# Kernel tuning notes

Hardware: AMD Instinct MI355X
Metric: run time of the kernel (lower is better)

Reference implementation:

```python
import jax, jax.numpy as jnp
import numpy as np

S, B, D, H = 512, 16, 512, 8  # seq_len, batch, d_model, n_heads
DH = D // H


def setup_inputs() -> dict:
    key = jax.random.key(0)
    k1, k2, k3, k4, k5 = jax.random.split(key, 5)
    x = jax.random.normal(k1, (S, B, D), dtype=jnp.float32)
    # nn.MultiheadAttention params: packed in_proj [3D, D], out_proj [D, D]
    W_in = jax.random.normal(k2, (3 * D, D), dtype=jnp.float32) * (D ** -0.5)
    b_in = jax.random.normal(k3, (3 * D,), dtype=jnp.float32) * 0.02
    W_out = jax.random.normal(k4, (D, D), dtype=jnp.float32) * (D ** -0.5)
    b_out = jax.random.normal(k5, (D,), dtype=jnp.float32) * 0.02
    return {"x": x, "W_in": W_in, "b_in": b_in, "W_out": W_out, "b_out": b_out}


def _mha(q_in, k_in, v_in, W_in, b_in, W_out, b_out):
    """torch.nn.MultiheadAttention (batch_first=False, eval mode). Inputs: (S, B, D)."""
    Wq, Wk, Wv = jnp.split(W_in, 3, axis=0)
    bq, bk, bv = jnp.split(b_in, 3)

    def heads(t):  # (S, B, D) -> (B, H, S, DH)
        s, b, _ = t.shape
        return t.reshape(s, b, H, DH).transpose(1, 2, 0, 3)

    q = heads(q_in @ Wq.T + bq) * (DH ** -0.5)
    k = heads(k_in @ Wk.T + bk)
    v = heads(v_in @ Wv.T + bv)
    attn = jax.nn.softmax(jnp.einsum('bhsd,bhtd->bhst', q, k), axis=-1)
    o = jnp.einsum('bhst,bhtd->bhsd', attn, v)          # (B, H, S, DH)
    o = o.transpose(2, 0, 1, 3).reshape(q_in.shape)      # (S, B, D)
    return o @ W_out.T + b_out


def reference(x, W_in, b_in, W_out, b_out):
    ch = jnp.arange(x.shape[-1])  # channel indices of last dim

    def step(acc, i):
        # x_i: only channel i kept (mirrors x_i[..., i] = x[..., i])
        x_i = jnp.where(ch == i, x, 0.0)
        # x_i_prime = where(x_i == 0, x, 0): x with channel i zeroed (where nonzero)
        x_ip = jnp.where(x_i == 0.0, x, 0.0)
        out = _mha(x_i, x_ip, x_ip, W_in, b_in, W_out, b_out)
        return acc + out, None

    # loop runs x.size(1) times, exactly as the torch code
    acc, _ = jax.lax.scan(step, jnp.zeros_like(x), jnp.arange(x.shape[1]))
    return acc
```

## Files before the change

kernel.cpp:

```cpp
#include <hip/hip_runtime.h>

#define S_LEN 512
#define BATCH 16
#define DMODEL 512
#define NHEAD 8
#define DH 64
#define NI 16

typedef float f32x4 __attribute__((ext_vector_type(4)));
typedef float f32x2 __attribute__((ext_vector_type(2)));
typedef short s16x8 __attribute__((ext_vector_type(8)));

__device__ __forceinline__ unsigned short f2bf(float f){
  unsigned int u = __float_as_uint(f);
  u += 0x7FFFu + ((u >> 16) & 1u);
  return (unsigned short)(u >> 16);
}

__device__ __forceinline__ void async16(const unsigned short* g, unsigned short* l){
  __builtin_amdgcn_global_load_lds(
      (const __attribute__((address_space(1))) unsigned int*)g,
      (__attribute__((address_space(3))) unsigned int*)l, 16, 0, 0);
}

template<int CTRL>
__device__ __forceinline__ float dppAdd(float x){
  int v = __builtin_amdgcn_update_dpp(0, __float_as_int(x), CTRL, 0xF, 0xF, true);
  return x + __int_as_float(v);
}

__device__ __forceinline__ void plswap32(float &a, float &b){
  asm("v_permlane32_swap_b32 %0, %1" : "+v"(a), "+v"(b));
}
__device__ __forceinline__ void plswap16(float &a, float &b){
  asm("v_permlane16_swap_b32 %0, %1" : "+v"(a), "+v"(b));
}
__device__ __forceinline__ unsigned int cvtpk_bf16(float lo, float hi){
  unsigned int r;
  asm("v_cvt_pk_bf16_f32 %0, %1, %2" : "=v"(r) : "v"(lo), "v"(hi));
  return r;
}

__global__ void k_prep(const float* __restrict__ x, unsigned short* __restrict__ xb,
                       float* __restrict__ zcol){
  int tid = blockIdx.x * 256 + threadIdx.x;
  float4 v = reinterpret_cast<const float4*>(x)[tid];
  ushort4 o;
  o.x = f2bf(v.x); o.y = f2bf(v.y); o.z = f2bf(v.z); o.w = f2bf(v.w);
  reinterpret_cast<ushort4*>(xb)[tid] = o;
  int d0 = (tid & 127) * 4;
  if (d0 < 16){
    int row = tid >> 7;
    int t = row >> 4, b = row & 15;
    zcol[(size_t)(b * 16 + d0 + 0) * 512 + t] = v.x;
    zcol[(size_t)(b * 16 + d0 + 1) * 512 + t] = v.y;
    zcol[(size_t)(b * 16 + d0 + 2) * 512 + t] = v.z;
    zcol[(size_t)(b * 16 + d0 + 3) * 512 + t] = v.w;
  }
}

__global__ void k_wcvt(const float* __restrict__ Win, const float* __restrict__ Wout,
                       unsigned short* __restrict__ Winb, unsigned short* __restrict__ Wob){
  int bidx = blockIdx.x;
  if (bidx < 768){
    int t = bidx * 256 + threadIdx.x;
    float4 v = reinterpret_cast<const float4*>(Win)[t];
    ushort4 o;
    o.x = f2bf(v.x); o.y = f2bf(v.y); o.z = f2bf(v.z); o.w = f2bf(v.w);
    reinterpret_cast<ushort4*>(Winb)[t] = o;
  } else {
    int t = (bidx - 768) * 256 + threadIdx.x;
    float4 v = reinterpret_cast<const float4*>(Wout)[t];
    ushort4 o;
    o.x = f2bf(v.x); o.y = f2bf(v.y); o.z = f2bf(v.z); o.w = f2bf(v.w);
    reinterpret_cast<ushort4*>(Wob)[t] = o;
  }
}

__global__ __launch_bounds__(256) void k_kv2(const unsigned short* __restrict__ xb,
    const unsigned short* __restrict__ Winb, const float* __restrict__ b_in,
    float* __restrict__ Kf, unsigned short* __restrict__ Vfb){
  __shared__ unsigned short As[2][128 * 32];
  __shared__ unsigned short Bs[2][128 * 32];
  int tid = threadIdx.x;
  int w = tid >> 6, l = tid & 63;
  int ln = l & 15, kb = l >> 4;
  int wr = w >> 1, wc = w & 1;
  int m0 = blockIdx.x * 128;
  int n0 = blockIdx.y * 128;
  const unsigned short* Brow = Winb + (size_t)512 * DMODEL;

  f32x4 acc[4][4];
  #pragma unroll
  for (int mi = 0; mi < 4; ++mi)
    #pragma unroll
    for (int nj = 0; nj < 4; ++nj) acc[mi][nj] = (f32x4){0.f,0.f,0.f,0.f};

  int c0 = tid, c1 = 256 + tid;
  int r0 = c0 >> 2, q0 = c0 & 3, r1 = c1 >> 2, q1 = c1 & 3;
  int lb0 = (w * 64) * 8, lb1 = (256 + w * 64) * 8;

  #define STAGE_KV(kt, buf) do { int k0 = (kt) * 32;                                   \
    async16(xb   + (size_t)(m0 + r0) * DMODEL + k0 + q0 * 8, &As[buf][lb0]);           \
    async16(xb   + (size_t)(m0 + r1) * DMODEL + k0 + q1 * 8, &As[buf][lb1]);           \
    async16(Brow + (size_t)(n0 + r0) * DMODEL + k0 + q0 * 8, &Bs[buf][lb0]);           \
    async16(Brow + (size_t)(n0 + r1) * DMODEL + k0 + q1 * 8, &Bs[buf][lb1]);           \
  } while(0)

  STAGE_KV(0, 0);
  __syncthreads();
  int cur = 0;
  for (int kt = 0; kt < 16; ++kt){
    if (kt < 15) STAGE_KV(kt + 1, cur ^ 1);
    const unsigned short* Ab = &As[cur][(wr * 64 + ln) * 32 + kb * 8];
    const unsigned short* Bb = &Bs[cur][(wc * 64 + ln) * 32 + kb * 8];
    s16x8 af[4], bf[4];
    #pragma unroll
    for (int mi = 0; mi < 4; ++mi) af[mi] = *reinterpret_cast<const s16x8*>(Ab + mi * 16 * 32);
    #pragma unroll
    for (int nj = 0; nj < 4; ++nj) bf[nj] = *reinterpret_cast<const s16x8*>(Bb + nj * 16 * 32);
    #pragma unroll
    for (int mi = 0; mi < 4; ++mi)
      #pragma unroll
      for (int nj = 0; nj < 4; ++nj)
        acc[mi][nj] = __builtin_amdgcn_mfma_f32_16x16x32_bf16(af[mi], bf[nj], acc[mi][nj], 0, 0, 0);
    __syncthreads();
    cur ^= 1;
  }
  #undef STAGE_KV

  #pragma unroll
  for (int nj = 0; nj < 4; ++nj){
    int n = n0 + wc * 64 + nj * 16 + ln;
    float bias = b_in[512 + n];
    #pragma unroll
    for (int mi = 0; mi < 4; ++mi){
      #pragma unroll
      for (int r = 0; r < 4; ++r){
        int m = m0 + wr * 64 + mi * 16 + kb * 4 + r;
        float v = acc[mi][nj][r] + bias;
        if (n < DMODEL) Kf[(size_t)m * DMODEL + n] = v;
        else            Vfb[(size_t)m * DMODEL + (n - DMODEL)] = f2bf(v);
      }
    }
  }
}

__global__ void k_tr(const unsigned short* __restrict__ Vfb, unsigned short* __restrict__ VfT){
  __shared__ unsigned short tile[32][34];
  int b = blockIdx.z; int t0 = blockIdx.x * 32; int d0 = blockIdx.y * 32;
  int tx = threadIdx.x & 31, ty = threadIdx.x >> 5;
  #pragma unroll
  for (int k = 0; k < 4; ++k){
    int row = ty + 8 * k;
    tile[row][tx] = Vfb[(size_t)((t0 + row) * BATCH + b) * DMODEL + d0 + tx];
  }
  __syncthreads();
  #pragma unroll
  for (int k = 0; k < 4; ++k){
    int row = ty + 8 * k;
    VfT[(size_t)b * (DMODEL * S_LEN) + (size_t)(d0 + row) * S_LEN + t0 + tx] = tile[tx][row];
  }
}

__global__ __launch_bounds__(256) void k_gh(const float* __restrict__ W_in,
    const float* __restrict__ b_in, const float* __restrict__ Kf,
    const float* __restrict__ zcol, float* __restrict__ G, float* __restrict__ H){
  const float SCALE = 0.18033688011112042f;
  int bh = blockIdx.x >> 1, th = blockIdx.x & 1;
  int b = bh >> 3, h = bh & 7;
  __shared__ float u[64][17];
  __shared__ float cvec[64];
  __shared__ float alpha[16], beta[16];
  int tid = threadIdx.x;
  for (int idx = tid; idx < 1024; idx += 256){
    int d = idx >> 4, i = idx & 15;
    u[d][i] = W_in[(size_t)(h * 64 + d) * DMODEL + i];
  }
  if (tid < 64) cvec[tid] = b_in[h * 64 + tid];
  __syncthreads();
  if (tid < 16){
    float a = 0.f, be = 0.f;
    for (int d = 0; d < 64; ++d){
      float wk = W_in[(size_t)(512 + h * 64 + d) * DMODEL + tid];
      a  += u[d][tid] * wk;
      be += cvec[d] * wk;
    }
    alpha[tid] = a; beta[tid] = be;
  }
  __syncthreads();
  int t = th * 256 + tid;
  float K[64];
  const float* kp = Kf + (size_t)(t * BATCH + b) * DMODEL + h * 64;
  #pragma unroll
  for (int d = 0; d < 64; d += 4){
    float4 v = *reinterpret_cast<const float4*>(kp + d);
    K[d] = v.x; K[d+1] = v.y; K[d+2] = v.z; K[d+3] = v.w;
  }
  float Bt = 0.f;
  #pragma unroll
  for (int d = 0; d < 64; ++d) Bt += cvec[d] * K[d];
  for (int i = 0; i < 16; ++i){
    float A = 0.f;
    #pragma unroll
    for (int d = 0; d < 64; ++d) A += u[d][i] * K[d];
    float z = zcol[(size_t)(b * 16 + i) * 512 + t];
    G[(size_t)(bh * 16 + i) * 512 + t] = (A  - alpha[i] * z) * SCALE;
    H[(size_t)(bh * 16 + i) * 512 + t] = (Bt - beta[i]  * z) * SCALE;
  }
}

__global__ __launch_bounds__(512, 2) void k_smpv(const float* __restrict__ G,
    const float* __restrict__ H, const float* __restrict__ zcol,
    const unsigned short* __restrict__ VfT, const float* __restrict__ W_in,
    unsigned short* __restrict__ Ob){
  __shared__ unsigned short Pl[32 * 512];
  __shared__ float Rs[32][17];
  __shared__ float Wvl[64][17];
  int j = blockIdx.x;
  int xcd = j & 7, rest = j >> 3;
  int bh_hi = rest & 15, sb = rest >> 4;
  int bh = bh_hi * 8 + xcd;
  int b = bh >> 3, h = bh & 7;
  int tid = threadIdx.x, w = tid >> 6, l = tid & 63;

  for (int idx = tid; idx < 1024; idx += 512){
    int d = idx >> 4, i = idx & 15;
    Wvl[d][i] = W_in[(size_t)(2 * DMODEL + h * 64 + d) * DMODEL + i];
  }

  const float* gb = G    + ((size_t)bh * NI) * S_LEN;
  const float* hb = H    + ((size_t)bh * NI) * S_LEN;
  const float* zb = zcol + ((size_t)b  * NI) * S_LEN;
  int t0 = l * 4, t1 = 256 + l * 4;
  int s_w = sb * 32 + w * 4;

  f32x2 Pacc[4][4];
  #pragma unroll
  for (int r = 0; r < 4; ++r)
    #pragma unroll
    for (int jp = 0; jp < 4; ++jp) Pacc[r][jp] = (f32x2){0.f, 0.f};

  for (int i = 0; i < NI; ++i){
    const float* gp = gb + (i << 9);
    const float* hp = hb + (i << 9);
    const float* zp = zb + (i << 9);
    f32x4 gA = *reinterpret_cast<const f32x4*>(gp + t0);
    f32x4 gB = *reinterpret_cast<const f32x4*>(gp + t1);
    f32x4 hA = *reinterpret_cast<const f32x4*>(hp + t0);
    f32x4 hB = *reinterpret_cast<const f32x4*>(hp + t1);
    f32x4 zA = *reinterpret_cast<const f32x4*>(zp + t0);
    f32x4 zB = *reinterpret_cast<const f32x4*>(zp + t1);
    float4 y4 = *reinterpret_cast<const float4*>(zp + s_w);
    f32x2 g2[4] = {gA.lo, gA.hi, gB.lo, gB.hi};
    f32x2 h2[4] = {hA.lo, hA.hi, hB.lo, hB.hi};
    f32x2 z2[4] = {zA.lo, zA.hi, zB.lo, zB.hi};
    float ys[4] = {y4.x, y4.y, y4.z, y4.w};

    f32x2 E[4][4];
    float pd[4], pr[4];
    #pragma unroll
    for (int r = 0; r < 4; ++r){
      f32x2 yv = {ys[r], ys[r]};
      f32x2 dacc = {0.f, 0.f}, racc = {0.f, 0.f};
      #pragma unroll
      for (int jp = 0; jp < 4; ++jp){
        f32x2 a = yv * g2[jp] + h2[jp];
        f32x2 e;
        e.x = __builtin_amdgcn_exp2f(a.x);
        e.y = __builtin_amdgcn_exp2f(a.y);
        asm volatile("" : "+v"(e));
        E[r][jp] = e;
        dacc += e;
        racc += e * z2[jp];
      }
      pd[r] = dacc.x + dacc.y;
      pr[r] = racc.x + racc.y;
    }

    plswap32(pd[0], pd[2]);  float dq0 = pd[0] + pd[2];
    plswap32(pd[1], pd[3]);  float dq1 = pd[1] + pd[3];
    plswap32(pr[0], pr[2]);  float rq0 = pr[0] + pr[2];
    plswap32(pr[1], pr[3]);  float rq1 = pr[1] + pr[3];
    plswap16(dq0, dq1);      float du = dq0 + dq1;
    plswap16(rq0, rq1);      float ru = rq0 + rq1;
    du = dppAdd<0x140>(du); ru = dppAdd<0x140>(ru);
    du = dppAdd<0x141>(du); ru = dppAdd<0x141>(ru);
    du = dppAdd<0x4E>(du);  ru = dppAdd<0x4E>(ru);
    du = dppAdd<0xB1>(du);  ru = dppAdd<0xB1>(ru);
    float inv = __builtin_amdgcn_rcpf(du);
    if ((l & 15) == 0)
      Rs[w * 4 + (l >> 4)][i] = ru * inv;
    #pragma unroll
    for (int r = 0; r < 4; ++r){
      float ir = __int_as_float(__builtin_amdgcn_readlane(__float_as_int(inv), 16 * r));
      f32x2 iv = {ir, ir};
      #pragma unroll
      for (int jp = 0; jp < 4; ++jp) Pacc[r][jp] += E[r][jp] * iv;
    }
  }

  #pragma unroll
  for (int r = 0; r < 4; ++r){
    int sl = w * 4 + r;
    unsigned int u0 = cvtpk_bf16(Pacc[r][0].x, Pacc[r][0].y);
    unsigned int u1 = cvtpk_bf16(Pacc[r][1].x, Pacc[r][1].y);
    unsigned int u2 = cvtpk_bf16(Pacc[r][2].x, Pacc[r][2].y);
    unsigned int u3 = cvtpk_bf16(Pacc[r][3].x, Pacc[r][3].y);
    int xr = (sl & 7) << 4;
    char* rowp = (char*)Pl + sl * 1024;
    uint2 v01; v01.x = u0; v01.y = u1;
    uint2 v23; v23.x = u2; v23.y = u3;
    *reinterpret_cast<uint2*>(rowp + ((l * 8) ^ xr)) = v01;
    *reinterpret_cast<uint2*>(rowp + ((512 + l * 8) ^ xr)) = v23;
  }
  __syncthreads();

  int ln = l & 15, kb = l >> 4;
  int sh = (w & 1) * 16;
  int dt = (w >> 1) * 16;
  const unsigned short* bp = VfT + (size_t)b * (DMODEL * S_LEN)
                             + (size_t)(h * 64 + dt + ln) * S_LEN + kb * 8;
  char* arow = (char*)Pl + (sh + ln) * 1024;
  int xa = (ln & 7) << 4;
  f32x4 acc = {0.f, 0.f, 0.f, 0.f};
  #pragma unroll
  for (int kt = 0; kt < 16; ++kt){
    s16x8 af = *reinterpret_cast<const s16x8*>(arow + ((kt * 64 + kb * 16) ^ xa));
    s16x8 bf = *reinterpret_cast<const s16x8*>(bp + kt * 32);
    acc = __builtin_amdgcn_mfma_f32_16x16x32_bf16(af, bf, acc, 0, 0, 0);
  }
  #pragma unroll
  for (int r = 0; r < 4; ++r){
    int sl = sh + kb * 4 + r;
    float corr = 0.f;
    #pragma unroll
    for (int i = 0; i < 16; ++i) corr += Rs[sl][i] * Wvl[dt + ln][i];
    float v = acc[r] - corr;
    int m = sb * 32 + sl;
    Ob[(size_t)(m * BATCH + b) * DMODEL + h * 64 + dt + ln] = f2bf(v);
  }
}

__global__ __launch_bounds__(256) void k_out2(const unsigned short* __restrict__ Ob,
    const unsigned short* __restrict__ Wob, const float* __restrict__ b_out,
    float* __restrict__ out){
  __shared__ unsigned short As[2][128 * 32];
  __shared__ unsigned short Bs[2][128 * 32];
  int tid = threadIdx.x;
  int w = tid >> 6, l = tid & 63;
  int ln = l & 15, kb = l >> 4;
  int wr = w >> 1, wc = w & 1;
  int m0 = blockIdx.x * 128;
  int n0 = blockIdx.y * 128;

  f32x4 acc[4][4];
  #pragma unroll
  for (int mi = 0; mi < 4; ++mi)
    #pragma unroll
    for (int nj = 0; nj < 4; ++nj) acc[mi][nj] = (f32x4){0.f,0.f,0.f,0.f};

  int c0 = tid, c1 = 256 + tid;
  int r0 = c0 >> 2, q0 = c0 & 3, r1 = c1 >> 2, q1 = c1 & 3;
  int lb0 = (w * 64) * 8, lb1 = (256 + w * 64) * 8;

  #define STAGE_O(kt, buf) do { int k0 = (kt) * 32;                                    \
    async16(Ob  + (size_t)(m0 + r0) * DMODEL + k0 + q0 * 8, &As[buf][lb0]);            \
    async16(Ob  + (size_t)(m0 + r1) * DMODEL + k0 + q1 * 8, &As[buf][lb1]);            \
    async16(Wob + (size_t)(n0 + r0) * DMODEL + k0 + q0 * 8, &Bs[buf][lb0]);            \
    async16(Wob + (size_t)(n0 + r1) * DMODEL + k0 + q1 * 8, &Bs[buf][lb1]);            \
  } while(0)

  STAGE_O(0, 0);
  __syncthreads();
  int cur = 0;
  for (int kt = 0; kt < 16; ++kt){
    if (kt < 15) STAGE_O(kt + 1, cur ^ 1);
    const unsigned short* Ab = &As[cur][(wr * 64 + ln) * 32 + kb * 8];
    const unsigned short* Bb = &Bs[cur][(wc * 64 + ln) * 32 + kb * 8];
    s16x8 af[4], bf[4];
    #pragma unroll
    for (int mi = 0; mi < 4; ++mi) af[mi] = *reinterpret_cast<const s16x8*>(Ab + mi * 16 * 32);
    #pragma unroll
    for (int nj = 0; nj < 4; ++nj) bf[nj] = *reinterpret_cast<const s16x8*>(Bb + nj * 16 * 32);
    #pragma unroll
    for (int mi = 0; mi < 4; ++mi)
      #pragma unroll
      for (int nj = 0; nj < 4; ++nj)
        acc[mi][nj] = __builtin_amdgcn_mfma_f32_16x16x32_bf16(af[mi], bf[nj], acc[mi][nj], 0, 0, 0);
    __syncthreads();
    cur ^= 1;
  }
  #undef STAGE_O

  #pragma unroll
  for (int nj = 0; nj < 4; ++nj){
    int n = n0 + wc * 64 + nj * 16 + ln;
    float bias = 16.0f * b_out[n];
    #pragma unroll
    for (int mi = 0; mi < 4; ++mi){
      #pragma unroll
      for (int r = 0; r < 4; ++r){
        int m = m0 + wr * 64 + mi * 16 + kb * 4 + r;
        out[(size_t)m * DMODEL + n] = acc[mi][nj][r] + bias;
      }
    }
  }
}

extern "C" void kernel_launch(void* const* d_in, const int* in_sizes, int n_in,
                              void* d_out, int out_size, void* d_ws, size_t ws_size,
                              hipStream_t stream) {
  const float* x     = (const float*)d_in[0];
  const float* W_in  = (const float*)d_in[1];
  const float* b_in  = (const float*)d_in[2];
  const float* W_out = (const float*)d_in[3];
  const float* b_out = (const float*)d_in[4];
  float* out = (float*)d_out;

  size_t off = 0;
  char* base = (char*)d_ws;
  auto alloc = [&](size_t bytes) -> void* {
    void* p = base + off;
    off += (bytes + 255) & ~(size_t)255;
    return p;
  };
  unsigned short* xb   = (unsigned short*)alloc(8388608);
  unsigned short* Winb = (unsigned short*)alloc(1572864);
  unsigned short* Wob  = (unsigned short*)alloc(524288);
  float*          zcol = (float*)alloc(524288);
  float*          Kf   = (float*)alloc(16777216);
  unsigned short* Vfb  = (unsigned short*)alloc(8388608);
  unsigned short* VfT  = (unsigned short*)alloc(8388608);
  float*          G    = (float*)alloc(4194304);
  float*          H    = (float*)alloc(4194304);
  unsigned short* Ob   = (unsigned short*)alloc(8388608);

  k_prep<<<4096, 256, 0, stream>>>(x, xb, zcol);
  k_wcvt<<<1024, 256, 0, stream>>>(W_in, W_out, Winb, Wob);

  { dim3 g(64, 8); k_kv2<<<g, 256, 0, stream>>>(xb, Winb, b_in, Kf, Vfb); }
  { dim3 g(16, 16, 16); k_tr<<<g, 256, 0, stream>>>(Vfb, VfT); }
  k_gh<<<256, 256, 0, stream>>>(W_in, b_in, Kf, zcol, G, H);

  k_smpv<<<2048, 512, 0, stream>>>(G, H, zcol, VfT, W_in, Ob);

  { dim3 g(64, 4); k_out2<<<g, 256, 0, stream>>>(Ob, Wob, b_out, out); }
}
```

Before: 181.4 us.

## Merge prep and weight-convert kernels, use packed FMA asm in softmax loop

Folds the x-to-bf16 prep kernel and the weight-conversion kernel into a single launch by extending the block range, which saves one kernel launch and its gap. In k_smpv the exp/accumulate loop now uses explicit v_pk_fma_f32/v_pk_add_f32 inline asm in place of compiler-generated vector arithmetic, and the empty asm barrier is dropped. The occupancy hint in launch_bounds (min 2 blocks) is also removed, which lets the compiler use more registers but may lower occupancy.

Measured after the change: 183.1 us. Within noise of the previous version (+0.9%).

```diff
diff --git a/kernel.cpp b/kernel.cpp
--- a/kernel.cpp
+++ b/kernel.cpp
@@ -40,36 +40,45 @@
   asm("v_cvt_pk_bf16_f32 %0, %1, %2" : "=v"(r) : "v"(lo), "v"(hi));
   return r;
 }
+__device__ __forceinline__ f32x2 pk_fma(f32x2 a, f32x2 b, f32x2 c){
+  f32x2 d;
+  asm("v_pk_fma_f32 %0, %1, %2, %3" : "=v"(d) : "v"(a), "v"(b), "v"(c));
+  return d;
+}
+__device__ __forceinline__ f32x2 pk_add(f32x2 a, f32x2 b){
+  f32x2 d;
+  asm("v_pk_add_f32 %0, %1, %2" : "=v"(d) : "v"(a), "v"(b));
+  return d;
+}
 
 __global__ void k_prep(const float* __restrict__ x, unsigned short* __restrict__ xb,
-                       float* __restrict__ zcol){
-  int tid = blockIdx.x * 256 + threadIdx.x;
-  float4 v = reinterpret_cast<const float4*>(x)[tid];
-  ushort4 o;
-  o.x = f2bf(v.x); o.y = f2bf(v.y); o.z = f2bf(v.z); o.w = f2bf(v.w);
-  reinterpret_cast<ushort4*>(xb)[tid] = o;
-  int d0 = (tid & 127) * 4;
-  if (d0 < 16){
-    int row = tid >> 7;
-    int t = row >> 4, b = row & 15;
-    zcol[(size_t)(b * 16 + d0 + 0) * 512 + t] = v.x;
-    zcol[(size_t)(b * 16 + d0 + 1) * 512 + t] = v.y;
-    zcol[(size_t)(b * 16 + d0 + 2) * 512 + t] = v.z;
-    zcol[(size_t)(b * 16 + d0 + 3) * 512 + t] = v.w;
-  }
-}
-
-__global__ void k_wcvt(const float* __restrict__ Win, const float* __restrict__ Wout,
-                       unsigned short* __restrict__ Winb, unsigned short* __restrict__ Wob){
+                       float* __restrict__ zcol, const float* __restrict__ Win,
+                       const float* __restrict__ Wout, unsigned short* __restrict__ Winb,
+                       unsigned short* __restrict__ Wob){
   int bidx = blockIdx.x;
-  if (bidx < 768){
-    int t = bidx * 256 + threadIdx.x;
+  if (bidx < 4096){
+    int tid = bidx * 256 + threadIdx.x;
+    float4 v = reinterpret_cast<const float4*>(x)[tid];
+    ushort4 o;
+    o.x = f2bf(v.x); o.y = f2bf(v.y); o.z = f2bf(v.z); o.w = f2bf(v.w);
+    reinterpret_cast<ushort4*>(xb)[tid] = o;
+    int d0 = (tid & 127) * 4;
+    if (d0 < 16){
+      int row = tid >> 7;
+      int t = row >> 4, b = row & 15;
+      zcol[(size_t)(b * 16 + d0 + 0) * 512 + t] = v.x;
+      zcol[(size_t)(b * 16 + d0 + 1) * 512 + t] = v.y;
+      zcol[(size_t)(b * 16 + d0 + 2) * 512 + t] = v.z;
+      zcol[(size_t)(b * 16 + d0 + 3) * 512 + t] = v.w;
+    }
+  } else if (bidx < 4864){
+    int t = (bidx - 4096) * 256 + threadIdx.x;
     float4 v = reinterpret_cast<const float4*>(Win)[t];
     ushort4 o;
     o.x = f2bf(v.x); o.y = f2bf(v.y); o.z = f2bf(v.z); o.w = f2bf(v.w);
     reinterpret_cast<ushort4*>(Winb)[t] = o;
   } else {
-    int t = (bidx - 768) * 256 + threadIdx.x;
+    int t = (bidx - 4864) * 256 + threadIdx.x;
     float4 v = reinterpret_cast<const float4*>(Wout)[t];
     ushort4 o;
     o.x = f2bf(v.x); o.y = f2bf(v.y); o.z = f2bf(v.z); o.w = f2bf(v.w);
@@ -210,7 +219,7 @@
   }
 }
 
-__global__ __launch_bounds__(512, 2) void k_smpv(const float* __restrict__ G,
+__global__ __launch_bounds__(512) void k_smpv(const float* __restrict__ G,
     const float* __restrict__ H, const float* __restrict__ zcol,
     const unsigned short* __restrict__ VfT, const float* __restrict__ W_in,
     unsigned short* __restrict__ Ob){
@@ -265,14 +274,13 @@
       f32x2 dacc = {0.f, 0.f}, racc = {0.f, 0.f};
       #pragma unroll
       for (int jp = 0; jp < 4; ++jp){
-        f32x2 a = yv * g2[jp] + h2[jp];
+        f32x2 a = pk_fma(yv, g2[jp], h2[jp]);
         f32x2 e;
         e.x = __builtin_amdgcn_exp2f(a.x);
         e.y = __builtin_amdgcn_exp2f(a.y);
-        asm volatile("" : "+v"(e));
         E[r][jp] = e;
-        dacc += e;
-        racc += e * z2[jp];
+        dacc = pk_add(dacc, e);
+        racc = pk_fma(e, z2[jp], racc);
       }
       pd[r] = dacc.x + dacc.y;
       pr[r] = racc.x + racc.y;
@@ -296,7 +304,7 @@
       float ir = __int_as_float(__builtin_amdgcn_readlane(__float_as_int(inv), 16 * r));
       f32x2 iv = {ir, ir};
       #pragma unroll
-      for (int jp = 0; jp < 4; ++jp) Pacc[r][jp] += E[r][jp] * iv;
+      for (int jp = 0; jp < 4; ++jp) Pacc[r][jp] = pk_fma(E[r][jp], iv, Pacc[r][jp]);
     }
   }
 
@@ -436,8 +444,7 @@
   float*          H    = (float*)alloc(4194304);
   unsigned short* Ob   = (unsigned short*)alloc(8388608);
 
-  k_prep<<<4096, 256, 0, stream>>>(x, xb, zcol);
-  k_wcvt<<<1024, 256, 0, stream>>>(W_in, W_out, Winb, Wob);
+  k_prep<<<5120, 256, 0, stream>>>(x, xb, zcol, W_in, W_out, Winb, Wob);
 
   { dim3 g(64, 8); k_kv2<<<g, 256, 0, stream>>>(xb, Winb, b_in, Kf, Vfb); }
   { dim3 g(16, 16, 16); k_tr<<<g, 256, 0, stream>>>(Vfb, VfT); }
```
